# Kernel optimization log

Hardware: AMD Instinct MI355X
Metric: run time of the kernel (lower is better)

Reference implementation:

```python
import jax, jax.numpy as jnp
import numpy as np

B, N = 1, 1024
C_A, C_Z, H = 768, 128, 16
CH = C_A // H  # 48
INV_SQRT_CH = float(1.0 / np.sqrt(CH))


def _ln(x, w, b):
    # torch.nn.LayerNorm over last dim, eps=1e-5
    m = jnp.mean(x, axis=-1, keepdims=True)
    v = jnp.mean(jnp.square(x - m), axis=-1, keepdims=True)
    return (x - m) * jax.lax.rsqrt(v + 1e-5) * w + b


def setup_inputs() -> dict:
    key = jax.random.key(0)
    ks = jax.random.split(key, 8)
    rn = lambda k, shape, sc: jax.random.normal(k, shape, dtype=jnp.float32) * sc
    return {
        "a": rn(ks[0], (B, N, C_A), 1.0),
        "z": rn(ks[1], (B, N, N, C_Z), 1.0),
        "mask": jnp.ones((B, N), dtype=jnp.float32),
        "ln_a_w": jnp.ones((C_A,), jnp.float32),
        "ln_a_b": jnp.zeros((C_A,), jnp.float32),
        "ln_z_w": jnp.ones((C_Z,), jnp.float32),
        "ln_z_b": jnp.zeros((C_Z,), jnp.float32),
        "Wq": rn(ks[2], (C_A, H * CH), 0.02),
        "bq": jnp.zeros((H * CH,), jnp.float32),
        "Wk": rn(ks[3], (C_A, H * CH), 0.02),
        "Wv": rn(ks[4], (C_A, H * CH), 0.02),
        "Wb": rn(ks[5], (C_Z, H), 0.02),
        "Wg": rn(ks[6], (C_A, H * CH), 0.02),
        "Wo": rn(ks[7], (H * CH, C_A), 0.02),
    }


def reference(a, z, mask, ln_a_w, ln_a_b, ln_z_w, ln_z_b, Wq, bq, Wk, Wv, Wb, Wg, Wo):
    an = _ln(a, ln_a_w, ln_a_b)                                  # [B, N, C_A]
    q = (an @ Wq + bq).reshape(B, N, H, CH)
    k = (an @ Wk).reshape(B, N, H, CH)
    v = (an @ Wv).reshape(B, N, H, CH)
    # pair bias: LayerNorm(z) -> per-head scalar bias [B, N, N, H]
    bpair = _ln(z, ln_z_w, ln_z_b) @ Wb
    mbias = (mask - 1.0)[:, None, None, :] * 1e9                  # [B, 1, 1, N]
    logits = jnp.einsum('bqhc,bkhc->bhqk', q, k) * INV_SQRT_CH
    logits = logits + jnp.transpose(bpair, (0, 3, 1, 2)) + mbias  # [B, H, N, N]
    attn = jax.nn.softmax(logits, axis=-1)
    o = jnp.einsum('bhqk,bkhc->bqhc', attn, v)                    # [B, N, H, CH]
    g = jax.nn.sigmoid(an @ Wg).reshape(B, N, H, CH)
    out = (g * o).reshape(B, N, H * CH) @ Wo                      # [B, N, C_A]
    return out
```

## Files before the change

### kernel.cpp

```cpp
#include <hip/hip_runtime.h>

#define NSEQ 1024
#define CA   768
#define CZ   128
#define NH   16
#define CHD  48
#define HC   768
#define INV_SQRT_CH 0.14433756729740643f

typedef float v4f __attribute__((ext_vector_type(4)));
typedef short v8s __attribute__((ext_vector_type(8)));

__device__ __forceinline__ short f2bf(float f) {
  union { float f; unsigned u; } v; v.f = f;
  unsigned r = v.u + 0x7fffu + ((v.u >> 16) & 1u);
  return (short)(r >> 16);
}
__device__ __forceinline__ float bf2f(short s) {
  union { unsigned u; float f; } v;
  v.u = ((unsigned)(unsigned short)s) << 16;
  return v.f;
}
__device__ __forceinline__ unsigned pack2(float a, float b) {
  return (unsigned)(unsigned short)f2bf(a) |
         ((unsigned)(unsigned short)f2bf(b) << 16);
}

__global__ __launch_bounds__(256) void k0_prep(
    const float* __restrict__ lnw, const float* __restrict__ lnb,
    const float* __restrict__ Wb, short* __restrict__ wWp,
    float* __restrict__ S1bW)
{
  const int t = threadIdx.x;
  const int s = t >> 6, l = t & 63;
  const int r16 = l & 15, cg = l >> 4;
  float v[8];
  #pragma unroll
  for (int j = 0; j < 8; ++j) {
    int d = s * 32 + cg * 8 + j;
    v[j] = lnw[d] * Wb[d * NH + r16];
  }
  uint4 pk;
  pk.x = pack2(v[0], v[1]); pk.y = pack2(v[2], v[3]);
  pk.z = pack2(v[4], v[5]); pk.w = pack2(v[6], v[7]);
  *(uint4*)(wWp + (s * 64 + l) * 8) = pk;
  if (t < NH) {
    float s1 = 0.f, bw = 0.f;
    for (int d = 0; d < CZ; ++d) {
      float wb = Wb[d * NH + t];
      s1 += bf2f(f2bf(lnw[d] * wb));
      bw += lnb[d] * wb;
    }
    S1bW[t] = s1;
    S1bW[NH + t] = bw;
  }
}

__global__ __launch_bounds__(256) void kc_conv(
    const float* __restrict__ Wq, const float* __restrict__ Wk,
    const float* __restrict__ Wv, const float* __restrict__ Wg,
    const float* __restrict__ Wo, short* __restrict__ WT,
    short* __restrict__ WoT)
{
  __shared__ float tile[64][65];
  const int bid = blockIdx.x;
  const int mat = bid / 144, rem = bid % 144;
  const int tk = rem % 12, tn = rem / 12;
  const int k0 = tk * 64, n0 = tn * 64;
  const float* __restrict__ W =
      (mat == 0) ? Wq : (mat == 1) ? Wk : (mat == 2) ? Wv : (mat == 3) ? Wg : Wo;
  const float s = (mat == 0) ? INV_SQRT_CH : 1.f;
  const int t = threadIdx.x;
  const int rr = t >> 4, cc = (t & 15) * 4;
  #pragma unroll
  for (int r = 0; r < 4; ++r) {
    v4f v = *(const v4f*)(W + (size_t)(k0 + r * 16 + rr) * HC + n0 + cc);
    tile[r * 16 + rr][cc + 0] = v[0];
    tile[r * 16 + rr][cc + 1] = v[1];
    tile[r * 16 + rr][cc + 2] = v[2];
    tile[r * 16 + rr][cc + 3] = v[3];
  }
  __syncthreads();
  short* dst = (mat < 4) ? (WT + (size_t)mat * HC * CA) : WoT;
  #pragma unroll
  for (int r = 0; r < 4; ++r) {
    const int nr = r * 16 + rr;
    float t0 = tile[cc + 0][nr] * s;
    float t1 = tile[cc + 1][nr] * s;
    float t2 = tile[cc + 2][nr] * s;
    float t3 = tile[cc + 3][nr] * s;
    uint2 pk; pk.x = pack2(t0, t1); pk.y = pack2(t2, t3);
    *(uint2*)(dst + (size_t)(n0 + nr) * CA + k0 + cc) = pk;
  }
}

__global__ __launch_bounds__(256) void k1_ln_a(
    const float* __restrict__ a, const float* __restrict__ lnw,
    const float* __restrict__ lnb, short* __restrict__ anb)
{
  const int row = blockIdx.x;
  const int tid = threadIdx.x;
  const float* ar = a + (size_t)row * CA;
  float x[3];
  float s = 0.f, s2 = 0.f;
  #pragma unroll
  for (int i = 0; i < 3; ++i) {
    x[i] = ar[tid + i * 256];
    s += x[i]; s2 += x[i] * x[i];
  }
  #pragma unroll
  for (int off = 1; off < 64; off <<= 1) {
    s += __shfl_xor(s, off);
    s2 += __shfl_xor(s2, off);
  }
  __shared__ float red[8];
  const int wv = tid >> 6;
  if ((tid & 63) == 0) { red[wv] = s; red[4 + wv] = s2; }
  __syncthreads();
  s = red[0] + red[1] + red[2] + red[3];
  s2 = red[4] + red[5] + red[6] + red[7];
  const float m = s * (1.f / CA);
  const float var = s2 * (1.f / CA) - m * m;
  const float rs = rsqrtf(var + 1e-5f);
  #pragma unroll
  for (int i = 0; i < 3; ++i) {
    int c = tid + i * 256;
    anb[(size_t)row * CA + c] = f2bf((x[i] - m) * rs * lnw[c] + lnb[c]);
  }
}

__global__ __launch_bounds__(256) void k23_fused(
    const short* __restrict__ anb, const short* __restrict__ WT,
    const float* __restrict__ bq, const float* __restrict__ z,
    const short* __restrict__ wWp, const float* __restrict__ S1bW,
    short* __restrict__ qb, short* __restrict__ kb, short* __restrict__ vT,
    float* __restrict__ gbuf, short* __restrict__ bpair)
{
  __shared__ __align__(16) char smem[20480];
  const int tid = threadIdx.x;
  const int w = tid >> 6, l = tid & 63;
  const int r16 = l & 15, cg = l >> 4;

  if (blockIdx.x < 192) {
    const int bid = blockIdx.x;
    const int bm = bid & 7;
    const int bnb = bid >> 3;
    const int m0 = bm * 128, n0 = bnb * 128;
    const int wr = w >> 1, wc = w & 1;

    short* As = (short*)smem;
    short* Bs = (short*)(smem + 10240);

    const int strow = w * 16 + (l >> 2);
    const int scol = (l & 3) * 8;

    v4f acc[4][4];
    #pragma unroll
    for (int i = 0; i < 4; ++i)
      #pragma unroll
      for (int j = 0; j < 4; ++j)
        acc[i][j] = (v4f){0.f, 0.f, 0.f, 0.f};

    for (int k0 = 0; k0 < CA; k0 += 32) {
      v8s av0 = *(const v8s*)(anb + (size_t)(m0 + strow) * CA + k0 + scol);
      v8s av1 = *(const v8s*)(anb + (size_t)(m0 + 64 + strow) * CA + k0 + scol);
      v8s bv0 = *(const v8s*)(WT + (size_t)(n0 + strow) * CA + k0 + scol);
      v8s bv1 = *(const v8s*)(WT + (size_t)(n0 + 64 + strow) * CA + k0 + scol);
      __syncthreads();
      *(v8s*)(As + (size_t)strow * 40 + scol) = av0;
      *(v8s*)(As + (size_t)(64 + strow) * 40 + scol) = av1;
      *(v8s*)(Bs + (size_t)strow * 40 + scol) = bv0;
      *(v8s*)(Bs + (size_t)(64 + strow) * 40 + scol) = bv1;
      __syncthreads();
      v8s a[4], b[4];
      #pragma unroll
      for (int m = 0; m < 4; ++m)
        a[m] = *(const v8s*)(As + (wr * 64 + m * 16 + r16) * 40 + cg * 8);
      #pragma unroll
      for (int n = 0; n < 4; ++n)
        b[n] = *(const v8s*)(Bs + (wc * 64 + n * 16 + r16) * 40 + cg * 8);
      #pragma unroll
      for (int m = 0; m < 4; ++m)
        #pragma unroll
        for (int n = 0; n < 4; ++n)
          acc[m][n] = __builtin_amdgcn_mfma_f32_16x16x32_bf16(a[m], b[n], acc[m][n], 0, 0, 0);
    }

    const int matsel = n0 / HC;
    #pragma unroll
    for (int n = 0; n < 4; ++n) {
      const int nc = (n0 % HC) + wc * 64 + n * 16 + r16;
      const int rbase = m0 + wr * 64 + cg * 4;
      if (matsel == 0) {
        const float bqs = bq[nc] * INV_SQRT_CH;
        #pragma unroll
        for (int m = 0; m < 4; ++m)
          #pragma unroll
          for (int j = 0; j < 4; ++j)
            qb[(size_t)(rbase + m * 16 + j) * HC + nc] = f2bf(acc[m][n][j] + bqs);
      } else if (matsel == 1) {
        #pragma unroll
        for (int m = 0; m < 4; ++m)
          #pragma unroll
          for (int j = 0; j < 4; ++j)
            kb[(size_t)(rbase + m * 16 + j) * HC + nc] = f2bf(acc[m][n][j]);
      } else if (matsel == 2) {
        #pragma unroll
        for (int m = 0; m < 4; ++m) {
          uint2 pk;
          pk.x = pack2(acc[m][n][0], acc[m][n][1]);
          pk.y = pack2(acc[m][n][2], acc[m][n][3]);
          *(uint2*)(vT + (size_t)nc * NSEQ + rbase + m * 16) = pk;
        }
      } else {
        #pragma unroll
        for (int m = 0; m < 4; ++m)
          #pragma unroll
          for (int j = 0; j < 4; ++j)
            gbuf[(size_t)(rbase + m * 16 + j) * HC + nc] =
                1.f / (1.f + __expf(-acc[m][n][j]));
      }
    }
  } else {
    const int zbid = blockIdx.x - 192;
    const int q = zbid >> 4;
    const int k0 = (zbid & 15) << 6;
    short* blds = (short*)smem;

    v8s bfrag[4];
    #pragma unroll
    for (int s = 0; s < 4; ++s) bfrag[s] = *(const v8s*)(wWp + (s * 64 + l) * 8);
    const float S1 = S1bW[r16];
    const float bW = S1bW[NH + r16];

    const int krow = k0 + w * 16 + r16;
    const float* __restrict__ zr = z + ((size_t)q * NSEQ + krow) * CZ;
    float sum = 0.f, sum2 = 0.f;
    v8s afrag[4];
    #pragma unroll
    for (int s = 0; s < 4; ++s) {
      v4f z0 = *(const v4f*)(zr + s * 32 + cg * 8);
      v4f z1 = *(const v4f*)(zr + s * 32 + cg * 8 + 4);
      v8s f;
      #pragma unroll
      for (int j = 0; j < 4; ++j) {
        sum += z0[j] + z1[j];
        sum2 += z0[j] * z0[j] + z1[j] * z1[j];
        f[j] = f2bf(z0[j]);
        f[j + 4] = f2bf(z1[j]);
      }
      afrag[s] = f;
    }
    sum  += __shfl_xor(sum, 16);  sum  += __shfl_xor(sum, 32);
    sum2 += __shfl_xor(sum2, 16); sum2 += __shfl_xor(sum2, 32);
    const float mean = sum * (1.f / CZ);
    const float var = sum2 * (1.f / CZ) - mean * mean;
    const float rs = rsqrtf(var + 1e-5f);

    v4f acc = {0.f, 0.f, 0.f, 0.f};
    #pragma unroll
    for (int s = 0; s < 4; ++s)
      acc = __builtin_amdgcn_mfma_f32_16x16x32_bf16(afrag[s], bfrag[s], acc, 0, 0, 0);

    #pragma unroll
    for (int j = 0; j < 4; ++j) {
      int src = cg * 4 + j;
      float mj = __shfl(mean, src);
      float rj = __shfl(rs, src);
      float bias = rj * (acc[j] - mj * S1) + bW;
      blds[r16 * 72 + w * 16 + cg * 4 + j] = f2bf(bias);
    }
    __syncthreads();
    const int h = tid >> 4, kk = (tid & 15) << 2;
    uint2 v = *(const uint2*)&blds[h * 72 + kk];
    *(uint2*)(bpair + (size_t)h * NSEQ * NSEQ + (size_t)q * NSEQ + k0 + kk) = v;
  }
}

__global__ __launch_bounds__(256) void k4_attn(
    const short* __restrict__ qb, const short* __restrict__ kb,
    const short* __restrict__ vT, const short* __restrict__ bpair,
    const float* __restrict__ mask,
    float* __restrict__ po, float* __restrict__ pm, float* __restrict__ plo)
{
  const int h = blockIdx.x & 15;
  const int qt = (blockIdx.x >> 4) & 15;
  const int ks = blockIdx.x >> 8;
  const int tid = threadIdx.x;
  const int w = tid >> 6, l = tid & 63;
  const int r16 = l & 15, cg = l >> 4;
  const int q0 = qt * 64 + w * 16;
  const int kstart = ks * 256;

  __shared__ __align__(16) short plds[4][16 * 40];
  short* pl = &plds[w][0];

  const v8s vzero = {0, 0, 0, 0, 0, 0, 0, 0};
  v8s qf0, qf1;
  {
    const short* qp = qb + (size_t)(q0 + r16) * HC + h * CHD;
    qf0 = *(const v8s*)(qp + cg * 8);
    qf1 = (cg < 2) ? *(const v8s*)(qp + 32 + cg * 8) : vzero;
  }
  v4f of0 = {0, 0, 0, 0}, of1 = {0, 0, 0, 0}, of2 = {0, 0, 0, 0};
  float mrun[4], lrun[4];
  #pragma unroll
  for (int j = 0; j < 4; ++j) { mrun[j] = -1e30f; lrun[j] = 0.f; }

  const size_t bpb = (size_t)h * NSEQ * NSEQ;

  for (int k0 = kstart; k0 < kstart + 256; k0 += 32) {
    v4f cs0 = {0, 0, 0, 0}, cs1 = {0, 0, 0, 0};
    {
      const short* kp = kb + (size_t)(k0 + r16) * HC + h * CHD;
      v8s b0 = *(const v8s*)(kp + cg * 8);
      v8s b1 = (cg < 2) ? *(const v8s*)(kp + 32 + cg * 8) : vzero;
      cs0 = __builtin_amdgcn_mfma_f32_16x16x32_bf16(qf0, b0, cs0, 0, 0, 0);
      cs0 = __builtin_amdgcn_mfma_f32_16x16x32_bf16(qf1, b1, cs0, 0, 0, 0);
    }
    {
      const short* kp = kb + (size_t)(k0 + 16 + r16) * HC + h * CHD;
      v8s b0 = *(const v8s*)(kp + cg * 8);
      v8s b1 = (cg < 2) ? *(const v8s*)(kp + 32 + cg * 8) : vzero;
      cs1 = __builtin_amdgcn_mfma_f32_16x16x32_bf16(qf0, b0, cs1, 0, 0, 0);
      cs1 = __builtin_amdgcn_mfma_f32_16x16x32_bf16(qf1, b1, cs1, 0, 0, 0);
    }
    float sv0[4], sv1[4];
    {
      const int kc0 = k0 + r16, kc1 = k0 + 16 + r16;
      const float mb0 = (mask[kc0] - 1.f) * 1e9f;
      const float mb1 = (mask[kc1] - 1.f) * 1e9f;
      #pragma unroll
      for (int j = 0; j < 4; ++j) {
        size_t qo = bpb + (size_t)(q0 + cg * 4 + j) * NSEQ;
        sv0[j] = cs0[j] + bf2f(bpair[qo + kc0]) + mb0;
        sv1[j] = cs1[j] + bf2f(bpair[qo + kc1]) + mb1;
      }
    }
    #pragma unroll
    for (int j = 0; j < 4; ++j) {
      float mx = fmaxf(sv0[j], sv1[j]);
      mx = fmaxf(mx, __shfl_xor(mx, 1));
      mx = fmaxf(mx, __shfl_xor(mx, 2));
      mx = fmaxf(mx, __shfl_xor(mx, 4));
      mx = fmaxf(mx, __shfl_xor(mx, 8));
      float mnew = fmaxf(mrun[j], mx);
      float alpha = __expf(mrun[j] - mnew);
      mrun[j] = mnew;
      float p0 = __expf(sv0[j] - mnew);
      float p1 = __expf(sv1[j] - mnew);
      float rsum = p0 + p1;
      rsum += __shfl_xor(rsum, 1);
      rsum += __shfl_xor(rsum, 2);
      rsum += __shfl_xor(rsum, 4);
      rsum += __shfl_xor(rsum, 8);
      lrun[j] = lrun[j] * alpha + rsum;
      of0[j] *= alpha; of1[j] *= alpha; of2[j] *= alpha;
      const int rr = (cg * 4 + j) * 40;
      pl[rr + r16] = f2bf(p0);
      pl[rr + 16 + r16] = f2bf(p1);
    }
    asm volatile("s_waitcnt lgkmcnt(0)" ::: "memory");
    __builtin_amdgcn_sched_barrier(0);
    v8s pa = *(const v8s*)(pl + r16 * 40 + cg * 8);
    {
      const short* vp = vT + (size_t)(h * CHD + r16) * NSEQ + k0 + cg * 8;
      v8s bv0 = *(const v8s*)vp;
      v8s bv1 = *(const v8s*)(vp + 16 * NSEQ);
      v8s bv2 = *(const v8s*)(vp + 32 * NSEQ);
      of0 = __builtin_amdgcn_mfma_f32_16x16x32_bf16(pa, bv0, of0, 0, 0, 0);
      of1 = __builtin_amdgcn_mfma_f32_16x16x32_bf16(pa, bv1, of1, 0, 0, 0);
      of2 = __builtin_amdgcn_mfma_f32_16x16x32_bf16(pa, bv2, of2, 0, 0, 0);
    }
  }
  #pragma unroll
  for (int j = 0; j < 4; ++j) {
    const int q = q0 + cg * 4 + j;
    const size_t rb = (((size_t)ks * NSEQ + q) * NH + h) * CHD + r16;
    po[rb]      = of0[j];
    po[rb + 16] = of1[j];
    po[rb + 32] = of2[j];
    if (r16 == 0) {
      pm[((size_t)ks * NSEQ + q) * NH + h] = mrun[j];
      plo[((size_t)ks * NSEQ + q) * NH + h] = lrun[j];
    }
  }
}

__global__ __launch_bounds__(256) void kcomb(
    const float* __restrict__ po, const float* __restrict__ pm,
    const float* __restrict__ plo, const float* __restrict__ gbuf,
    short* __restrict__ gob)
{
  const int q = blockIdx.x;
  const int t = threadIdx.x;
  const int h = t >> 4, s = t & 15;
  float mi[4], li[4];
  #pragma unroll
  for (int i = 0; i < 4; ++i) {
    mi[i] = pm[((size_t)i * NSEQ + q) * NH + h];
    li[i] = plo[((size_t)i * NSEQ + q) * NH + h];
  }
  float mstar = fmaxf(fmaxf(mi[0], mi[1]), fmaxf(mi[2], mi[3]));
  float wgt[4], L = 0.f;
  #pragma unroll
  for (int i = 0; i < 4; ++i) { wgt[i] = __expf(mi[i] - mstar); L += li[i] * wgt[i]; }
  const float inv = 1.f / L;
  #pragma unroll
  for (int dd = 0; dd < 3; ++dd) {
    const int d = s + dd * 16;
    float o = 0.f;
    #pragma unroll
    for (int i = 0; i < 4; ++i)
      o += po[(((size_t)i * NSEQ + q) * NH + h) * CHD + d] * wgt[i];
    const float gv = gbuf[(size_t)q * HC + h * CHD + d];
    gob[(size_t)q * HC + h * CHD + d] = f2bf(o * inv * gv);
  }
}

__global__ __launch_bounds__(256) void k5_out(
    const short* __restrict__ gob, const short* __restrict__ WoT,
    float* __restrict__ out)
{
  __shared__ __align__(16) short As[128 * 40];
  __shared__ __align__(16) short Bs[128 * 40];
  const int tid = threadIdx.x;
  const int w = tid >> 6, l = tid & 63;
  const int r16 = l & 15, cg = l >> 4;
  const int bm = blockIdx.x & 7;
  const int bn = blockIdx.x >> 3;
  const int m0 = bm * 128, n0 = bn * 128;
  const int wr = w >> 1, wc = w & 1;
  const int strow = w * 16 + (l >> 2);
  const int scol = (l & 3) * 8;

  v4f acc[4][4];
  #pragma unroll
  for (int i = 0; i < 4; ++i)
    #pragma unroll
    for (int j = 0; j < 4; ++j)
      acc[i][j] = (v4f){0.f, 0.f, 0.f, 0.f};

  for (int k0 = 0; k0 < CA; k0 += 32) {
    v8s av0 = *(const v8s*)(gob + (size_t)(m0 + strow) * CA + k0 + scol);
    v8s av1 = *(const v8s*)(gob + (size_t)(m0 + 64 + strow) * CA + k0 + scol);
    v8s bv0 = *(const v8s*)(WoT + (size_t)(n0 + strow) * CA + k0 + scol);
    v8s bv1 = *(const v8s*)(WoT + (size_t)(n0 + 64 + strow) * CA + k0 + scol);
    __syncthreads();
    *(v8s*)(As + (size_t)strow * 40 + scol) = av0;
    *(v8s*)(As + (size_t)(64 + strow) * 40 + scol) = av1;
    *(v8s*)(Bs + (size_t)strow * 40 + scol) = bv0;
    *(v8s*)(Bs + (size_t)(64 + strow) * 40 + scol) = bv1;
    __syncthreads();
    v8s a[4], b[4];
    #pragma unroll
    for (int m = 0; m < 4; ++m)
      a[m] = *(const v8s*)(As + (wr * 64 + m * 16 + r16) * 40 + cg * 8);
    #pragma unroll
    for (int n = 0; n < 4; ++n)
      b[n] = *(const v8s*)(Bs + (wc * 64 + n * 16 + r16) * 40 + cg * 8);
    #pragma unroll
    for (int m = 0; m < 4; ++m)
      #pragma unroll
      for (int n = 0; n < 4; ++n)
        acc[m][n] = __builtin_amdgcn_mfma_f32_16x16x32_bf16(a[m], b[n], acc[m][n], 0, 0, 0);
  }

  #pragma unroll
  for (int n = 0; n < 4; ++n) {
    const int nc = n0 + wc * 64 + n * 16 + r16;
    const int rbase = m0 + wr * 64 + cg * 4;
    #pragma unroll
    for (int m = 0; m < 4; ++m)
      #pragma unroll
      for (int j = 0; j < 4; ++j)
        out[(size_t)(rbase + m * 16 + j) * CA + nc] = acc[m][n][j];
  }
}

extern "C" void kernel_launch(void* const* d_in, const int* in_sizes, int n_in,
                              void* d_out, int out_size, void* d_ws, size_t ws_size,
                              hipStream_t stream) {
  const float* a      = (const float*)d_in[0];
  const float* z      = (const float*)d_in[1];
  const float* mask   = (const float*)d_in[2];
  const float* ln_a_w = (const float*)d_in[3];
  const float* ln_a_b = (const float*)d_in[4];
  const float* ln_z_w = (const float*)d_in[5];
  const float* ln_z_b = (const float*)d_in[6];
  const float* Wq     = (const float*)d_in[7];
  const float* bq     = (const float*)d_in[8];
  const float* Wk     = (const float*)d_in[9];
  const float* Wv     = (const float*)d_in[10];
  const float* Wb     = (const float*)d_in[11];
  const float* Wg     = (const float*)d_in[12];
  const float* Wo     = (const float*)d_in[13];
  float* out = (float*)d_out;

  char* ws = (char*)d_ws;
  short* anb   = (short*)(ws);
  short* WT    = (short*)(ws + (2ull << 20));
  short* WoT   = (short*)(ws + (7ull << 20));
  short* qb    = (short*)(ws + (9ull << 20));
  short* kb    = (short*)(ws + (11ull << 20));
  short* vT    = (short*)(ws + (13ull << 20));
  float* gbuf  = (float*)(ws + (15ull << 20));
  short* wWp   = (short*)(ws + (19ull << 20));
  float* S1bW  = (float*)(ws + (19ull << 20) + 4096ull);
  short* gob   = (short*)(ws + (20ull << 20));
  float* po    = (float*)(ws + (22ull << 20));
  float* pm    = (float*)(ws + (36ull << 20));
  float* plo   = (float*)(ws + (37ull << 20));
  short* bpair = (short*)(ws + (38ull << 20));

  k0_prep<<<1, 256, 0, stream>>>(ln_z_w, ln_z_b, Wb, wWp, S1bW);
  kc_conv<<<720, 256, 0, stream>>>(Wq, Wk, Wv, Wg, Wo, WT, WoT);
  k1_ln_a<<<1024, 256, 0, stream>>>(a, ln_a_w, ln_a_b, anb);
  k23_fused<<<192 + 16384, 256, 0, stream>>>(anb, WT, bq, z, wWp, S1bW,
                                             qb, kb, vT, gbuf, bpair);
  k4_attn<<<1024, 256, 0, stream>>>(qb, kb, vT, bpair, mask, po, pm, plo);
  kcomb<<<1024, 256, 0, stream>>>(po, pm, plo, gbuf, gob);
  k5_out<<<48, 256, 0, stream>>>(gob, WoT, out);
}
```

Baseline: 201.7 us.

## Merge prep kernels, use hardware bf16 pack, widen attention key chunks

Folds the three front kernels (pair-bias weight prep, weight transpose/convert, LayerNorm of a) into one launch dispatched by block index, which removes two launch gaps. Replaces the software round-to-nearest bf16 packing with the v_cvt_pk_bf16_f32 instruction in several places. The attention kernel now handles 128 keys per online-softmax step instead of 32, so there are fewer max/sum reductions and rescales, at the cost of more live registers and a larger P tile in LDS.

```diff
diff --git a/kernel.cpp b/kernel.cpp
--- a/kernel.cpp
+++ b/kernel.cpp
@@ -21,111 +21,105 @@
   v.u = ((unsigned)(unsigned short)s) << 16;
   return v.f;
 }
-__device__ __forceinline__ unsigned pack2(float a, float b) {
-  return (unsigned)(unsigned short)f2bf(a) |
-         ((unsigned)(unsigned short)f2bf(b) << 16);
-}
-
-__global__ __launch_bounds__(256) void k0_prep(
-    const float* __restrict__ lnw, const float* __restrict__ lnb,
-    const float* __restrict__ Wb, short* __restrict__ wWp,
-    float* __restrict__ S1bW)
-{
-  const int t = threadIdx.x;
-  const int s = t >> 6, l = t & 63;
-  const int r16 = l & 15, cg = l >> 4;
-  float v[8];
-  #pragma unroll
-  for (int j = 0; j < 8; ++j) {
-    int d = s * 32 + cg * 8 + j;
-    v[j] = lnw[d] * Wb[d * NH + r16];
-  }
-  uint4 pk;
-  pk.x = pack2(v[0], v[1]); pk.y = pack2(v[2], v[3]);
-  pk.z = pack2(v[4], v[5]); pk.w = pack2(v[6], v[7]);
-  *(uint4*)(wWp + (s * 64 + l) * 8) = pk;
-  if (t < NH) {
-    float s1 = 0.f, bw = 0.f;
-    for (int d = 0; d < CZ; ++d) {
-      float wb = Wb[d * NH + t];
-      s1 += bf2f(f2bf(lnw[d] * wb));
-      bw += lnb[d] * wb;
-    }
-    S1bW[t] = s1;
-    S1bW[NH + t] = bw;
-  }
-}
-
-__global__ __launch_bounds__(256) void kc_conv(
+__device__ __forceinline__ unsigned cvtpk(float lo, float hi) {
+  unsigned r;
+  asm("v_cvt_pk_bf16_f32 %0, %1, %2" : "=v"(r) : "v"(lo), "v"(hi));
+  return r;
+}
+
+__global__ __launch_bounds__(256) void k_front(
+    const float* __restrict__ lnzw, const float* __restrict__ lnzb,
+    const float* __restrict__ Wb, short* __restrict__ wWp, float* __restrict__ S1bW,
     const float* __restrict__ Wq, const float* __restrict__ Wk,
     const float* __restrict__ Wv, const float* __restrict__ Wg,
-    const float* __restrict__ Wo, short* __restrict__ WT,
-    short* __restrict__ WoT)
+    const float* __restrict__ Wo, short* __restrict__ WT, short* __restrict__ WoT,
+    const float* __restrict__ a, const float* __restrict__ lnaw,
+    const float* __restrict__ lnab, short* __restrict__ anb)
 {
-  __shared__ float tile[64][65];
+  __shared__ __align__(16) char fsm[64 * 65 * 4];
   const int bid = blockIdx.x;
-  const int mat = bid / 144, rem = bid % 144;
-  const int tk = rem % 12, tn = rem / 12;
-  const int k0 = tk * 64, n0 = tn * 64;
-  const float* __restrict__ W =
-      (mat == 0) ? Wq : (mat == 1) ? Wk : (mat == 2) ? Wv : (mat == 3) ? Wg : Wo;
-  const float s = (mat == 0) ? INV_SQRT_CH : 1.f;
   const int t = threadIdx.x;
-  const int rr = t >> 4, cc = (t & 15) * 4;
-  #pragma unroll
-  for (int r = 0; r < 4; ++r) {
-    v4f v = *(const v4f*)(W + (size_t)(k0 + r * 16 + rr) * HC + n0 + cc);
-    tile[r * 16 + rr][cc + 0] = v[0];
-    tile[r * 16 + rr][cc + 1] = v[1];
-    tile[r * 16 + rr][cc + 2] = v[2];
-    tile[r * 16 + rr][cc + 3] = v[3];
-  }
-  __syncthreads();
-  short* dst = (mat < 4) ? (WT + (size_t)mat * HC * CA) : WoT;
-  #pragma unroll
-  for (int r = 0; r < 4; ++r) {
-    const int nr = r * 16 + rr;
-    float t0 = tile[cc + 0][nr] * s;
-    float t1 = tile[cc + 1][nr] * s;
-    float t2 = tile[cc + 2][nr] * s;
-    float t3 = tile[cc + 3][nr] * s;
-    uint2 pk; pk.x = pack2(t0, t1); pk.y = pack2(t2, t3);
-    *(uint2*)(dst + (size_t)(n0 + nr) * CA + k0 + cc) = pk;
-  }
-}
-
-__global__ __launch_bounds__(256) void k1_ln_a(
-    const float* __restrict__ a, const float* __restrict__ lnw,
-    const float* __restrict__ lnb, short* __restrict__ anb)
-{
-  const int row = blockIdx.x;
-  const int tid = threadIdx.x;
-  const float* ar = a + (size_t)row * CA;
-  float x[3];
-  float s = 0.f, s2 = 0.f;
-  #pragma unroll
-  for (int i = 0; i < 3; ++i) {
-    x[i] = ar[tid + i * 256];
-    s += x[i]; s2 += x[i] * x[i];
-  }
-  #pragma unroll
-  for (int off = 1; off < 64; off <<= 1) {
-    s += __shfl_xor(s, off);
-    s2 += __shfl_xor(s2, off);
-  }
-  __shared__ float red[8];
-  const int wv = tid >> 6;
-  if ((tid & 63) == 0) { red[wv] = s; red[4 + wv] = s2; }
-  __syncthreads();
-  s = red[0] + red[1] + red[2] + red[3];
-  s2 = red[4] + red[5] + red[6] + red[7];
-  const float m = s * (1.f / CA);
-  const float var = s2 * (1.f / CA) - m * m;
-  const float rs = rsqrtf(var + 1e-5f);
-  #pragma unroll
-  for (int i = 0; i < 3; ++i) {
-    int c = tid + i * 256;
-    anb[(size_t)row * CA + c] = f2bf((x[i] - m) * rs * lnw[c] + lnb[c]);
+
+  if (bid == 0) {
+    const int s = t >> 6, l = t & 63;
+    const int r16 = l & 15, cg = l >> 4;
+    float v[8];
+    #pragma unroll
+    for (int j = 0; j < 8; ++j) {
+      int d = s * 32 + cg * 8 + j;
+      v[j] = lnzw[d] * Wb[d * NH + r16];
+    }
+    uint4 pk;
+    pk.x = cvtpk(v[0], v[1]); pk.y = cvtpk(v[2], v[3]);
+    pk.z = cvtpk(v[4], v[5]); pk.w = cvtpk(v[6], v[7]);
+    *(uint4*)(wWp + (s * 64 + l) * 8) = pk;
+    if (t < NH) {
+      float s1 = 0.f, bw = 0.f;
+      for (int d = 0; d < CZ; ++d) {
+        float wb = Wb[d * NH + t];
+        s1 += bf2f(f2bf(lnzw[d] * wb));
+        bw += lnzb[d] * wb;
+      }
+      S1bW[t] = s1;
+      S1bW[NH + t] = bw;
+    }
+  } else if (bid <= 720) {
+    float (*tile)[65] = (float(*)[65])fsm;
+    const int cb = bid - 1;
+    const int mat = cb / 144, rem = cb % 144;
+    const int tk = rem % 12, tn = rem / 12;
+    const int k0 = tk * 64, n0 = tn * 64;
+    const float* __restrict__ W =
+        (mat == 0) ? Wq : (mat == 1) ? Wk : (mat == 2) ? Wv : (mat == 3) ? Wg : Wo;
+    const float s = (mat == 0) ? INV_SQRT_CH : 1.f;
+    const int rr = t >> 4, cc = (t & 15) * 4;
+    #pragma unroll
+    for (int r = 0; r < 4; ++r) {
+      v4f v = *(const v4f*)(W + (size_t)(k0 + r * 16 + rr) * HC + n0 + cc);
+      tile[r * 16 + rr][cc + 0] = v[0];
+      tile[r * 16 + rr][cc + 1] = v[1];
+      tile[r * 16 + rr][cc + 2] = v[2];
+      tile[r * 16 + rr][cc + 3] = v[3];
+    }
+    __syncthreads();
+    short* dst = (mat < 4) ? (WT + (size_t)mat * HC * CA) : WoT;
+    #pragma unroll
+    for (int r = 0; r < 4; ++r) {
+      const int nr = r * 16 + rr;
+      uint2 pk;
+      pk.x = cvtpk(tile[cc + 0][nr] * s, tile[cc + 1][nr] * s);
+      pk.y = cvtpk(tile[cc + 2][nr] * s, tile[cc + 3][nr] * s);
+      *(uint2*)(dst + (size_t)(n0 + nr) * CA + k0 + cc) = pk;
+    }
+  } else {
+    float* red = (float*)fsm;
+    const int row = bid - 721;
+    const float* ar = a + (size_t)row * CA;
+    float x[3];
+    float s = 0.f, s2 = 0.f;
+    #pragma unroll
+    for (int i = 0; i < 3; ++i) {
+      x[i] = ar[t + i * 256];
+      s += x[i]; s2 += x[i] * x[i];
+    }
+    #pragma unroll
+    for (int off = 1; off < 64; off <<= 1) {
+      s += __shfl_xor(s, off);
+      s2 += __shfl_xor(s2, off);
+    }
+    const int wv = t >> 6;
+    if ((t & 63) == 0) { red[wv] = s; red[4 + wv] = s2; }
+    __syncthreads();
+    s = red[0] + red[1] + red[2] + red[3];
+    s2 = red[4] + red[5] + red[6] + red[7];
+    const float m = s * (1.f / CA);
+    const float var = s2 * (1.f / CA) - m * m;
+    const float rs = rsqrtf(var + 1e-5f);
+    #pragma unroll
+    for (int i = 0; i < 3; ++i) {
+      int c = t + i * 256;
+      anb[(size_t)row * CA + c] = f2bf((x[i] - m) * rs * lnaw[c] + lnab[c]);
+    }
   }
 }
 
@@ -208,8 +202,8 @@
         #pragma unroll
         for (int m = 0; m < 4; ++m) {
           uint2 pk;
-          pk.x = pack2(acc[m][n][0], acc[m][n][1]);
-          pk.y = pack2(acc[m][n][2], acc[m][n][3]);
+          pk.x = cvtpk(acc[m][n][0], acc[m][n][1]);
+          pk.y = cvtpk(acc[m][n][2], acc[m][n][3]);
           *(uint2*)(vT + (size_t)nc * NSEQ + rbase + m * 16) = pk;
         }
       } else {
@@ -241,15 +235,17 @@
     for (int s = 0; s < 4; ++s) {
       v4f z0 = *(const v4f*)(zr + s * 32 + cg * 8);
       v4f z1 = *(const v4f*)(zr + s * 32 + cg * 8 + 4);
-      v8s f;
       #pragma unroll
       for (int j = 0; j < 4; ++j) {
         sum += z0[j] + z1[j];
         sum2 += z0[j] * z0[j] + z1[j] * z1[j];
-        f[j] = f2bf(z0[j]);
-        f[j + 4] = f2bf(z1[j]);
       }
-      afrag[s] = f;
+      union { v8s s8; unsigned u[4]; } fu;
+      fu.u[0] = cvtpk(z0[0], z0[1]);
+      fu.u[1] = cvtpk(z0[2], z0[3]);
+      fu.u[2] = cvtpk(z1[0], z1[1]);
+      fu.u[3] = cvtpk(z1[2], z1[3]);
+      afrag[s] = fu.s8;
     }
     sum  += __shfl_xor(sum, 16);  sum  += __shfl_xor(sum, 32);
     sum2 += __shfl_xor(sum2, 16); sum2 += __shfl_xor(sum2, 32);
@@ -262,14 +258,18 @@
     for (int s = 0; s < 4; ++s)
       acc = __builtin_amdgcn_mfma_f32_16x16x32_bf16(afrag[s], bfrag[s], acc, 0, 0, 0);
 
+    float bv[4];
     #pragma unroll
     for (int j = 0; j < 4; ++j) {
       int src = cg * 4 + j;
       float mj = __shfl(mean, src);
       float rj = __shfl(rs, src);
-      float bias = rj * (acc[j] - mj * S1) + bW;
-      blds[r16 * 72 + w * 16 + cg * 4 + j] = f2bf(bias);
-    }
+      bv[j] = rj * (acc[j] - mj * S1) + bW;
+    }
+    uint2 bu;
+    bu.x = cvtpk(bv[0], bv[1]);
+    bu.y = cvtpk(bv[2], bv[3]);
+    *(uint2*)&blds[r16 * 72 + w * 16 + cg * 4] = bu;
     __syncthreads();
     const int h = tid >> 4, kk = (tid & 15) << 2;
     uint2 v = *(const uint2*)&blds[h * 72 + kk];
@@ -277,6 +277,7 @@
   }
 }
 
+#define PL_STRIDE 136
 __global__ __launch_bounds__(256) void k4_attn(
     const short* __restrict__ qb, const short* __restrict__ kb,
     const short* __restrict__ vT, const short* __restrict__ bpair,
@@ -292,7 +293,7 @@
   const int q0 = qt * 64 + w * 16;
   const int kstart = ks * 256;
 
-  __shared__ __align__(16) short plds[4][16 * 40];
+  __shared__ __align__(16) short plds[4][16 * PL_STRIDE];
   short* pl = &plds[w][0];
 
   const v8s vzero = {0, 0, 0, 0, 0, 0, 0, 0};
@@ -309,62 +310,66 @@
 
   const size_t bpb = (size_t)h * NSEQ * NSEQ;
 
-  for (int k0 = kstart; k0 < kstart + 256; k0 += 32) {
-    v4f cs0 = {0, 0, 0, 0}, cs1 = {0, 0, 0, 0};
-    {
-      const short* kp = kb + (size_t)(k0 + r16) * HC + h * CHD;
+  #pragma unroll
+  for (int ch = 0; ch < 2; ++ch) {
+    const int k0 = kstart + ch * 128;
+
+    v4f cs[8];
+    #pragma unroll
+    for (int kt = 0; kt < 8; ++kt) {
+      const short* kp = kb + (size_t)(k0 + kt * 16 + r16) * HC + h * CHD;
       v8s b0 = *(const v8s*)(kp + cg * 8);
       v8s b1 = (cg < 2) ? *(const v8s*)(kp + 32 + cg * 8) : vzero;
-      cs0 = __builtin_amdgcn_mfma_f32_16x16x32_bf16(qf0, b0, cs0, 0, 0, 0);
-      cs0 = __builtin_amdgcn_mfma_f32_16x16x32_bf16(qf1, b1, cs0, 0, 0, 0);
-    }
-    {
-      const short* kp = kb + (size_t)(k0 + 16 + r16) * HC + h * CHD;
-      v8s b0 = *(const v8s*)(kp + cg * 8);
-      v8s b1 = (cg < 2) ? *(const v8s*)(kp + 32 + cg * 8) : vzero;
-      cs1 = __builtin_amdgcn_mfma_f32_16x16x32_bf16(qf0, b0, cs1, 0, 0, 0);
-      cs1 = __builtin_amdgcn_mfma_f32_16x16x32_bf16(qf1, b1, cs1, 0, 0, 0);
-    }
-    float sv0[4], sv1[4];
-    {
-      const int kc0 = k0 + r16, kc1 = k0 + 16 + r16;
-      const float mb0 = (mask[kc0] - 1.f) * 1e9f;
-      const float mb1 = (mask[kc1] - 1.f) * 1e9f;
+      v4f tacc = {0.f, 0.f, 0.f, 0.f};
+      tacc = __builtin_amdgcn_mfma_f32_16x16x32_bf16(qf0, b0, tacc, 0, 0, 0);
+      tacc = __builtin_amdgcn_mfma_f32_16x16x32_bf16(qf1, b1, tacc, 0, 0, 0);
+      cs[kt] = tacc;
+    }
+    #pragma unroll
+    for (int kt = 0; kt < 8; ++kt) {
+      const int kc = k0 + kt * 16 + r16;
+      const float mb = (mask[kc] - 1.f) * 1e9f;
       #pragma unroll
       for (int j = 0; j < 4; ++j) {
-        size_t qo = bpb + (size_t)(q0 + cg * 4 + j) * NSEQ;
-        sv0[j] = cs0[j] + bf2f(bpair[qo + kc0]) + mb0;
-        sv1[j] = cs1[j] + bf2f(bpair[qo + kc1]) + mb1;
+        const size_t qo = bpb + (size_t)(q0 + cg * 4 + j) * NSEQ;
+        cs[kt][j] += bf2f(bpair[qo + kc]) + mb;
       }
     }
     #pragma unroll
     for (int j = 0; j < 4; ++j) {
-      float mx = fmaxf(sv0[j], sv1[j]);
+      float mx = fmaxf(fmaxf(fmaxf(cs[0][j], cs[1][j]), fmaxf(cs[2][j], cs[3][j])),
+                       fmaxf(fmaxf(cs[4][j], cs[5][j]), fmaxf(cs[6][j], cs[7][j])));
       mx = fmaxf(mx, __shfl_xor(mx, 1));
       mx = fmaxf(mx, __shfl_xor(mx, 2));
       mx = fmaxf(mx, __shfl_xor(mx, 4));
       mx = fmaxf(mx, __shfl_xor(mx, 8));
-      float mnew = fmaxf(mrun[j], mx);
-      float alpha = __expf(mrun[j] - mnew);
+      const float mnew = fmaxf(mrun[j], mx);
+      const float alpha = __expf(mrun[j] - mnew);
       mrun[j] = mnew;
-      float p0 = __expf(sv0[j] - mnew);
-      float p1 = __expf(sv1[j] - mnew);
-      float rsum = p0 + p1;
+      float p[8];
+      #pragma unroll
+      for (int kt = 0; kt < 8; ++kt) p[kt] = __expf(cs[kt][j] - mnew);
+      float rsum = ((p[0] + p[1]) + (p[2] + p[3])) + ((p[4] + p[5]) + (p[6] + p[7]));
       rsum += __shfl_xor(rsum, 1);
       rsum += __shfl_xor(rsum, 2);
       rsum += __shfl_xor(rsum, 4);
       rsum += __shfl_xor(rsum, 8);
       lrun[j] = lrun[j] * alpha + rsum;
       of0[j] *= alpha; of1[j] *= alpha; of2[j] *= alpha;
-      const int rr = (cg * 4 + j) * 40;
-      pl[rr + r16] = f2bf(p0);
-      pl[rr + 16 + r16] = f2bf(p1);
+      const int rowb = (cg * 4 + j) * PL_STRIDE;
+      #pragma unroll
+      for (int t2 = 0; t2 < 4; ++t2) {
+        unsigned u = cvtpk(p[2 * t2], p[2 * t2 + 1]);
+        pl[rowb + (2 * t2) * 16 + r16] = (short)u;
+        pl[rowb + (2 * t2 + 1) * 16 + r16] = (short)(u >> 16);
+      }
     }
     asm volatile("s_waitcnt lgkmcnt(0)" ::: "memory");
     __builtin_amdgcn_sched_barrier(0);
-    v8s pa = *(const v8s*)(pl + r16 * 40 + cg * 8);
-    {
-      const short* vp = vT + (size_t)(h * CHD + r16) * NSEQ + k0 + cg * 8;
+    #pragma unroll
+    for (int ks4 = 0; ks4 < 4; ++ks4) {
+      v8s pa = *(const v8s*)(pl + r16 * PL_STRIDE + ks4 * 32 + cg * 8);
+      const short* vp = vT + (size_t)(h * CHD + r16) * NSEQ + k0 + ks4 * 32 + cg * 8;
       v8s bv0 = *(const v8s*)vp;
       v8s bv1 = *(const v8s*)(vp + 16 * NSEQ);
       v8s bv2 = *(const v8s*)(vp + 32 * NSEQ);
@@ -373,6 +378,7 @@
       of2 = __builtin_amdgcn_mfma_f32_16x16x32_bf16(pa, bv2, of2, 0, 0, 0);
     }
   }
+
   #pragma unroll
   for (int j = 0; j < 4; ++j) {
     const int q = q0 + cg * 4 + j;
@@ -513,9 +519,9 @@
   float* plo   = (float*)(ws + (37ull << 20));
   short* bpair = (short*)(ws + (38ull << 20));
 
-  k0_prep<<<1, 256, 0, stream>>>(ln_z_w, ln_z_b, Wb, wWp, S1bW);
-  kc_conv<<<720, 256, 0, stream>>>(Wq, Wk, Wv, Wg, Wo, WT, WoT);
-  k1_ln_a<<<1024, 256, 0, stream>>>(a, ln_a_w, ln_a_b, anb);
+  k_front<<<1745, 256, 0, stream>>>(ln_z_w, ln_z_b, Wb, wWp, S1bW,
+                                    Wq, Wk, Wv, Wg, Wo, WT, WoT,
+                                    a, ln_a_w, ln_a_b, anb);
   k23_fused<<<192 + 16384, 256, 0, stream>>>(anb, WT, bq, z, wWp, S1bW,
                                              qb, kb, vT, gbuf, bpair);
   k4_attn<<<1024, 256, 0, stream>>>(qb, kb, vT, bpair, mask, po, pm, plo);
```

After: 201.7 us. About the same (-0.0%).
